# Kernel tuning notes

Measured on AMD Instinct MI355X. Metric: run time of the kernel, lower is better.

The kernel has to match this reference:

```python
import jax, jax.numpy as jnp
import numpy as np

PATCH = 11
STRIDE = 2
WIN_SIGMA = 1.5
C1 = 0.01 ** 2
C2 = 0.03 ** 2


def gauss_win():
    # 1D gaussian (matches _fspecial_gauss_1d) outer-producted to a 2D window
    # over the p*p patch pixels (separable SSIM window), flattened to (p*p,).
    coords = jnp.arange(PATCH, dtype=jnp.float32) - PATCH // 2
    g = jnp.exp(-(coords ** 2) / (2.0 * WIN_SIGMA ** 2))
    g = g / g.sum()
    return jnp.outer(g, g).reshape(-1)


def extract_patches(im):
    # im: (B,3,H,W) -> (B, n_patches, 3, p*p); feature dim of
    # conv_general_dilated_patches is channel-major (C, p, p).
    pat = jax.lax.conv_general_dilated_patches(
        im, (PATCH, PATCH), (STRIDE, STRIDE), 'VALID')  # (B, 3*p*p, H', W')
    B = im.shape[0]
    pat = pat.reshape(B, 3, PATCH * PATCH, -1)
    return jnp.transpose(pat, (0, 3, 1, 2))


def mmd_ssim(xp, yp, win):
    # xp: (M,3,pp), yp: (N,3,pp). Returns scalar MMD = s^T K s, where
    # K is the pairwise SSIM kernel matrix and s the scale vector.
    M, N = xp.shape[0], yp.shape[0]
    s = jnp.concatenate([jnp.full((N,), 1.0 / N, jnp.float32),
                         jnp.full((M,), -1.0 / M, jnp.float32)])
    X = jnp.concatenate([xp, yp], axis=0)
    X = (X + 1.0) / 2.0
    Xw = X * win                                   # (P,3,pp)
    mus = Xw.sum(-1)                               # (P,3)
    mus_sq = mus ** 2
    sigmas = (Xw * X).sum(-1) - mus_sq             # (P,3)
    sig_sum = sigmas[:, None] + sigmas[None, :]    # (P,P,3)
    mus_sum = mus_sq[:, None] + mus_sq[None, :]
    mus_mult = mus_sq[:, None] * mus_sq[None, :]
    sigmas_xy = jnp.einsum('icp,jcp->ijc', Xw, X) - mus_mult
    cs_map = (2.0 * sigmas_xy + C2) / (sig_sum + C2)
    ssim_map = (2.0 * mus_mult + C1) / (mus_sum + C1) * cs_map
    K = ssim_map.mean(-1)                          # (P,P)
    return s @ (K @ s)


def setup_inputs() -> dict:
    key = jax.random.key(0)
    kx, ky = jax.random.split(key)
    x = jax.random.normal(kx, (2, 3, 80, 80), dtype=jnp.float32)
    y = jax.random.normal(ky, (2, 3, 80, 80), dtype=jnp.float32)
    return {"x": x, "y": y}


def reference(x, y):
    win = gauss_win()
    xp = extract_patches(x)  # (B, P, 3, pp)
    yp = extract_patches(y)
    losses = jax.vmap(lambda a, b: mmd_ssim(a, b, win))(xp, yp)  # (B,)
    return losses.mean()  # batch_reduction='mean'
```

## Files before the change

kernel.cpp:

```cpp
#include <hip/hip_runtime.h>
#include <math.h>

#define PATCH   11
#define PP      121
#define NPX     35
#define NPATCH  1225
#define P2      2450
#define NC      3
#define NB      2
#define TILE    64
#define NT      39
#define NTP     ((NT*(NT+1))/2)
#define NROW    (NT*TILE)
#define KP      128
#define C1f     1.0e-4f
#define C2f     9.0e-4f

typedef _Float16 f16;
typedef __attribute__((ext_vector_type(8)))  _Float16 f16x8;
typedef __attribute__((ext_vector_type(16))) float    f32x16;

__device__ __forceinline__ void gload16(const void* g, void* l) {
    __builtin_amdgcn_global_load_lds((const __attribute__((address_space(1))) void*)(g),
                                     (__attribute__((address_space(3))) void*)(l),
                                     16, 0, 0);
}

__global__ __launch_bounds__(256) void extract_kernel(
        const float* __restrict__ x, const float* __restrict__ y,
        f16* __restrict__ Zh, f16* __restrict__ Zl,
        float* __restrict__ musq, float* __restrict__ sig,
        double* __restrict__ acc) {
    int w = threadIdx.x >> 6, lane = threadIdx.x & 63;
    int i = blockIdx.x * 4 + w;
    int c = blockIdx.y, b = blockIdx.z;
    if (threadIdx.x == 0 && blockIdx.x == 0 && c == 0 && b == 0) acc[0] = 0.0;
    if (i >= NROW) return;

    size_t rowbase = ((size_t)(b * NC + c) * NROW + i) * (size_t)KP;
    f16* zh = Zh + rowbase;
    f16* zl = Zl + rowbase;
    size_t sidx = (size_t)(b * NC + c) * NROW + i;

    if (i >= P2) {
        ((unsigned int*)zh)[lane] = 0u;
        ((unsigned int*)zl)[lane] = 0u;
        if (lane == 0) { musq[sidx] = 0.f; sig[sidx] = 0.f; }
        return;
    }

    float g1[PATCH]; float gs = 0.f;
#pragma unroll
    for (int k = 0; k < PATCH; k++) {
        float d = (float)(k - PATCH / 2);
        g1[k] = expf(-(d * d) / (2.0f * 1.5f * 1.5f));
        gs += g1[k];
    }
    float inv = 1.0f / gs;
    float inv2 = inv * inv;

    const float* img = (i < NPATCH) ? x : y;
    int ip = (i < NPATCH) ? i : i - NPATCH;
    int py = ip / NPX, px = ip - py * NPX;
    const float* base = img + ((size_t)(b * NC + c) * 80 + py * 2) * 80 + px * 2;

    float mu = 0.f, e2 = 0.f;
    f16 hv[2], lv[2];
#pragma unroll
    for (int q = 0; q < 2; q++) {
        int p = lane + q * 64;
        float z = 0.f;
        if (p < PP) {
            int r = p / PATCH, s = p - (p / PATCH) * PATCH;
            float wgt = g1[r] * g1[s] * inv2;
            float X = (base[r * 80 + s] + 1.0f) * 0.5f;
            mu = fmaf(wgt, X, mu);
            e2 = fmaf(wgt * X, X, e2);
            z = sqrtf(wgt) * X;
        }
        hv[q] = (f16)z;
        lv[q] = (f16)(z - (float)hv[q]);
    }
    zh[lane]      = hv[0];
    zh[lane + 64] = hv[1];
    zl[lane]      = lv[0];
    zl[lane + 64] = lv[1];

#pragma unroll
    for (int off = 32; off > 0; off >>= 1) {
        mu += __shfl_down(mu, off);
        e2 += __shfl_down(e2, off);
    }
    if (lane == 0) {
        float m2 = mu * mu;
        musq[sidx] = m2;
        sig [sidx] = e2 - m2;
    }
}

__device__ __forceinline__ f16x8 frag(const f16* arr, int r, int kb) {
    int off = r * 256 + (kb ^ ((r & 15) << 4));
    return *(const f16x8*)((const char*)arr + off);
}

__global__ __launch_bounds__(256) void pair_kernel(
        const f16* __restrict__ Zh, const f16* __restrict__ Zl,
        const float* __restrict__ musq, const float* __restrict__ sig,
        double* __restrict__ acc) {
    __shared__ __align__(16) f16 lds[4 * TILE * KP];

    int t = threadIdx.x;
    int lane = t & 63, w = t >> 6;
    int b = blockIdx.y;

    int l = blockIdx.x, ti = 0;
    while (l >= NT - ti) { l -= NT - ti; ti++; }
    int tj = ti + l;

    f16* A_h = lds;
    f16* A_l = lds + 8192;
    f16* B_h = lds + 16384;
    f16* B_l = lds + 24576;

    int wr = w >> 1, wc = w & 1;
    int rA = wr * 32 + (lane & 31);
    int rB = wc * 32 + (lane & 31);
    int kb0 = (lane >> 5) * 16;

    int soff[4];
#pragma unroll
    for (int q = 0; q < 4; q++) {
        int U = (w * 4 + q) * 64 + lane;
        int r = U >> 4, u = U & 15;
        soff[q] = r * 256 + (u ^ (r & 15)) * 16;
    }

    double local = 0.0;

    for (int c = 0; c < NC; c++) {
        __syncthreads();
        const char* gAh = (const char*)(Zh + ((size_t)(b * NC + c) * NROW + ti * TILE) * KP);
        const char* gAl = (const char*)(Zl + ((size_t)(b * NC + c) * NROW + ti * TILE) * KP);
        const char* gBh = (const char*)(Zh + ((size_t)(b * NC + c) * NROW + tj * TILE) * KP);
        const char* gBl = (const char*)(Zl + ((size_t)(b * NC + c) * NROW + tj * TILE) * KP);
#pragma unroll
        for (int q = 0; q < 4; q++) {
            int ldo = (w * 4 + q) * 512;
            gload16(gAh + soff[q], A_h + ldo);
            gload16(gAl + soff[q], A_l + ldo);
            gload16(gBh + soff[q], B_h + ldo);
            gload16(gBl + soff[q], B_l + ldo);
        }
        __syncthreads();

        f32x16 acc2 = {};
#pragma unroll
        for (int ks = 0; ks < 8; ks++) {
            int kb = ks * 32 + kb0;
            f16x8 ah = frag(A_h, rA, kb);
            f16x8 bh = frag(B_h, rB, kb);
            f16x8 al = frag(A_l, rA, kb);
            f16x8 bl = frag(B_l, rB, kb);
            acc2 = __builtin_amdgcn_mfma_f32_32x32x16_f16(ah, bh, acc2, 0, 0, 0);
            acc2 = __builtin_amdgcn_mfma_f32_32x32x16_f16(ah, bl, acc2, 0, 0, 0);
            acc2 = __builtin_amdgcn_mfma_f32_32x32x16_f16(al, bh, acc2, 0, 0, 0);
        }

        const float* msq = musq + (size_t)(b * NC + c) * NROW;
        const float* sg  = sig  + (size_t)(b * NC + c) * NROW;
        int row0 = ti * TILE + wr * 32;
        int col0 = tj * TILE + wc * 32;
        int gj = col0 + (lane & 31);
        float mj = msq[gj], sj = sg[gj];
        bool yj = gj < NPATCH;
#pragma unroll
        for (int reg = 0; reg < 16; reg++) {
            int gi = row0 + (reg & 3) + 8 * (reg >> 2) + 4 * (lane >> 5);
            float mi = msq[gi], si = sg[gi];
            float G   = acc2[reg];
            float mm  = mi * mj;
            float sxy = G - mm;
            float num = (2.f * mm + C1f) * (2.f * sxy + C2f);
            float den = (mi + mj + C1f) * (si + sj + C2f);
            float kv  = num * __builtin_amdgcn_rcpf(den);
            float wgt;
            if (ti == tj) wgt = (gj > gi) ? 2.f : ((gj == gi) ? 1.f : 0.f);
            else          wgt = 2.f;
            if (gi >= P2 || gj >= P2) wgt = 0.f;
            float sgn = ((gi < NPATCH) == yj) ? 1.f : -1.f;
            local += (double)(wgt * sgn * kv);
        }
    }

    __syncthreads();
#pragma unroll
    for (int off = 32; off > 0; off >>= 1)
        local += __shfl_down(local, off);
    double* red = (double*)lds;
    if (lane == 0) red[w] = local;
    __syncthreads();
    if (t == 0)
        atomicAdd(acc, red[0] + red[1] + red[2] + red[3]);
}

__global__ void finalize_kernel(const double* __restrict__ acc,
                                float* __restrict__ out) {
    if (threadIdx.x == 0 && blockIdx.x == 0)
        out[0] = (float)(acc[0] * (1.0 / (2.0 * 3.0 * (double)NPATCH * (double)NPATCH)));
}

extern "C" void kernel_launch(void* const* d_in, const int* in_sizes, int n_in,
                              void* d_out, int out_size, void* d_ws, size_t ws_size,
                              hipStream_t stream) {
    const float* x = (const float*)d_in[0];
    const float* y = (const float*)d_in[1];
    float* out = (float*)d_out;

    double* acc = (double*)d_ws;
    f16* Zh = (f16*)((char*)d_ws + 16);
    size_t zcnt = (size_t)NB * NC * NROW * KP;
    f16* Zl = Zh + zcnt;
    float* musq = (float*)(Zl + zcnt);
    float* sig  = musq + (size_t)NB * NC * NROW;

    dim3 g1((NROW + 3) / 4, NC, NB);
    extract_kernel<<<g1, 256, 0, stream>>>(x, y, Zh, Zl, musq, sig, acc);

    dim3 g2(NTP, NB);
    pair_kernel<<<g2, 256, 0, stream>>>(Zh, Zl, musq, sig, acc);

    finalize_kernel<<<1, 64, 0, stream>>>(acc, out);
}
```

Measured before the change: 103.5 us.

## Drop LDS staging; use k-chunk-major layout with direct global fragment loads

```diff
diff --git a/kernel.cpp b/kernel.cpp
--- a/kernel.cpp
+++ b/kernel.cpp
@@ -8,11 +8,12 @@
 #define P2      2450
 #define NC      3
 #define NB      2
-#define TILE    64
-#define NT      39
-#define NTP     ((NT*(NT+1))/2)
-#define NROW    (NT*TILE)
-#define KP      128
+#define NROW    2560
+#define NKC     16
+#define RT      128
+#define CT      64
+#define NSTRIP  (NROW/RT)
+#define NCT     (NROW/CT)
 #define C1f     1.0e-4f
 #define C2f     9.0e-4f
 
@@ -20,183 +21,131 @@
 typedef __attribute__((ext_vector_type(8)))  _Float16 f16x8;
 typedef __attribute__((ext_vector_type(16))) float    f32x16;
 
-__device__ __forceinline__ void gload16(const void* g, void* l) {
-    __builtin_amdgcn_global_load_lds((const __attribute__((address_space(1))) void*)(g),
-                                     (__attribute__((address_space(3))) void*)(l),
-                                     16, 0, 0);
-}
-
 __global__ __launch_bounds__(256) void extract_kernel(
         const float* __restrict__ x, const float* __restrict__ y,
         f16* __restrict__ Zh, f16* __restrict__ Zl,
-        float* __restrict__ musq, float* __restrict__ sig,
-        double* __restrict__ acc) {
-    int w = threadIdx.x >> 6, lane = threadIdx.x & 63;
-    int i = blockIdx.x * 4 + w;
+        float2* __restrict__ msig, double* __restrict__ acc) {
+    int t = threadIdx.x, lane = t & 63, w = t >> 6;
+    int i  = blockIdx.x * 16 + w * 4 + (lane >> 4);
+    int kc = lane & 15;
     int c = blockIdx.y, b = blockIdx.z;
-    if (threadIdx.x == 0 && blockIdx.x == 0 && c == 0 && b == 0) acc[0] = 0.0;
-    if (i >= NROW) return;
+    if (t == 0 && blockIdx.x == 0 && c == 0 && b == 0) acc[0] = 0.0;
 
-    size_t rowbase = ((size_t)(b * NC + c) * NROW + i) * (size_t)KP;
-    f16* zh = Zh + rowbase;
-    f16* zl = Zl + rowbase;
-    size_t sidx = (size_t)(b * NC + c) * NROW + i;
-
-    if (i >= P2) {
-        ((unsigned int*)zh)[lane] = 0u;
-        ((unsigned int*)zl)[lane] = 0u;
-        if (lane == 0) { musq[sidx] = 0.f; sig[sidx] = 0.f; }
-        return;
-    }
+    int bc = b * NC + c;
+    bool valid = (i < P2);
 
     float g1[PATCH]; float gs = 0.f;
 #pragma unroll
     for (int k = 0; k < PATCH; k++) {
         float d = (float)(k - PATCH / 2);
-        g1[k] = expf(-(d * d) / (2.0f * 1.5f * 1.5f));
+        g1[k] = expf(-(d * d) / 4.5f);
         gs += g1[k];
     }
-    float inv = 1.0f / gs;
-    float inv2 = inv * inv;
+    float inv2 = 1.0f / (gs * gs);
 
-    const float* img = (i < NPATCH) ? x : y;
-    int ip = (i < NPATCH) ? i : i - NPATCH;
-    int py = ip / NPX, px = ip - py * NPX;
-    const float* base = img + ((size_t)(b * NC + c) * 80 + py * 2) * 80 + px * 2;
+    const float* base = x;
+    if (valid) {
+        const float* img = (i < NPATCH) ? x : y;
+        int ip = (i < NPATCH) ? i : i - NPATCH;
+        int py = ip / NPX, px = ip - py * NPX;
+        base = img + ((size_t)bc * 80 + py * 2) * 80 + px * 2;
+    }
 
     float mu = 0.f, e2 = 0.f;
-    f16 hv[2], lv[2];
+    f16x8 hv = {}, lv = {};
 #pragma unroll
-    for (int q = 0; q < 2; q++) {
-        int p = lane + q * 64;
+    for (int q = 0; q < 8; q++) {
+        int p = kc * 8 + q;
         float z = 0.f;
-        if (p < PP) {
+        if (valid && p < PP) {
             int r = p / PATCH, s = p - (p / PATCH) * PATCH;
-            float wgt = g1[r] * g1[s] * inv2;
+            float wg = g1[r] * g1[s] * inv2;
             float X = (base[r * 80 + s] + 1.0f) * 0.5f;
-            mu = fmaf(wgt, X, mu);
-            e2 = fmaf(wgt * X, X, e2);
-            z = sqrtf(wgt) * X;
+            mu = fmaf(wg, X, mu);
+            e2 = fmaf(wg * X, X, e2);
+            z = sqrtf(wg) * X;
         }
-        hv[q] = (f16)z;
-        lv[q] = (f16)(z - (float)hv[q]);
+        f16 h = (f16)z;
+        hv[q] = h;
+        lv[q] = (f16)(z - (float)h);
     }
-    zh[lane]      = hv[0];
-    zh[lane + 64] = hv[1];
-    zl[lane]      = lv[0];
-    zl[lane + 64] = lv[1];
+    size_t off = (((size_t)bc * NKC + kc) * NROW + i) * 8;
+    *(f16x8*)(Zh + off) = hv;
+    *(f16x8*)(Zl + off) = lv;
 
 #pragma unroll
-    for (int off = 32; off > 0; off >>= 1) {
-        mu += __shfl_down(mu, off);
-        e2 += __shfl_down(e2, off);
+    for (int m = 1; m < 16; m <<= 1) {
+        mu += __shfl_xor(mu, m);
+        e2 += __shfl_xor(e2, m);
     }
-    if (lane == 0) {
+    if (kc == 0) {
         float m2 = mu * mu;
-        musq[sidx] = m2;
-        sig [sidx] = e2 - m2;
+        msig[(size_t)bc * NROW + i] = make_float2(m2, e2 - m2);
     }
-}
-
-__device__ __forceinline__ f16x8 frag(const f16* arr, int r, int kb) {
-    int off = r * 256 + (kb ^ ((r & 15) << 4));
-    return *(const f16x8*)((const char*)arr + off);
 }
 
 __global__ __launch_bounds__(256) void pair_kernel(
         const f16* __restrict__ Zh, const f16* __restrict__ Zl,
-        const float* __restrict__ musq, const float* __restrict__ sig,
-        double* __restrict__ acc) {
-    __shared__ __align__(16) f16 lds[4 * TILE * KP];
+        const float2* __restrict__ msig, double* __restrict__ acc) {
+    int tj = blockIdx.x, si = blockIdx.y, b = blockIdx.z;
+    if (tj < 2 * si) return;
 
-    int t = threadIdx.x;
-    int lane = t & 63, w = t >> 6;
-    int b = blockIdx.y;
-
-    int l = blockIdx.x, ti = 0;
-    while (l >= NT - ti) { l -= NT - ti; ti++; }
-    int tj = ti + l;
-
-    f16* A_h = lds;
-    f16* A_l = lds + 8192;
-    f16* B_h = lds + 16384;
-    f16* B_l = lds + 24576;
-
-    int wr = w >> 1, wc = w & 1;
-    int rA = wr * 32 + (lane & 31);
-    int rB = wc * 32 + (lane & 31);
-    int kb0 = (lane >> 5) * 16;
-
-    int soff[4];
-#pragma unroll
-    for (int q = 0; q < 4; q++) {
-        int U = (w * 4 + q) * 64 + lane;
-        int r = U >> 4, u = U & 15;
-        soff[q] = r * 256 + (u ^ (r & 15)) * 16;
-    }
+    int t = threadIdx.x, lane = t & 63, w = t >> 6;
+    int lr = lane & 31, hi = lane >> 5;
+    int R0 = si * RT + w * 32;
 
     double local = 0.0;
 
     for (int c = 0; c < NC; c++) {
-        __syncthreads();
-        const char* gAh = (const char*)(Zh + ((size_t)(b * NC + c) * NROW + ti * TILE) * KP);
-        const char* gAl = (const char*)(Zl + ((size_t)(b * NC + c) * NROW + ti * TILE) * KP);
-        const char* gBh = (const char*)(Zh + ((size_t)(b * NC + c) * NROW + tj * TILE) * KP);
-        const char* gBl = (const char*)(Zl + ((size_t)(b * NC + c) * NROW + tj * TILE) * KP);
+        int bc = b * NC + c;
+        const f16* zh = Zh + (size_t)bc * NKC * NROW * 8;
+        const f16* zl = Zl + (size_t)bc * NKC * NROW * 8;
+        const float2* ms = msig + (size_t)bc * NROW;
+
+        f16x8 Ah[8];
 #pragma unroll
-        for (int q = 0; q < 4; q++) {
-            int ldo = (w * 4 + q) * 512;
-            gload16(gAh + soff[q], A_h + ldo);
-            gload16(gAl + soff[q], A_l + ldo);
-            gload16(gBh + soff[q], B_h + ldo);
-            gload16(gBl + soff[q], B_l + ldo);
-        }
-        __syncthreads();
+        for (int ks = 0; ks < 8; ks++)
+            Ah[ks] = *(const f16x8*)(zh + ((size_t)(ks * 2 + hi) * NROW + R0 + lr) * 8);
 
-        f32x16 acc2 = {};
 #pragma unroll
-        for (int ks = 0; ks < 8; ks++) {
-            int kb = ks * 32 + kb0;
-            f16x8 ah = frag(A_h, rA, kb);
-            f16x8 bh = frag(B_h, rB, kb);
-            f16x8 al = frag(A_l, rA, kb);
-            f16x8 bl = frag(B_l, rB, kb);
-            acc2 = __builtin_amdgcn_mfma_f32_32x32x16_f16(ah, bh, acc2, 0, 0, 0);
-            acc2 = __builtin_amdgcn_mfma_f32_32x32x16_f16(ah, bl, acc2, 0, 0, 0);
-            acc2 = __builtin_amdgcn_mfma_f32_32x32x16_f16(al, bh, acc2, 0, 0, 0);
-        }
+        for (int cb = 0; cb < 2; cb++) {
+            int C0 = tj * CT + cb * 32;
+            f32x16 a = {};
+#pragma unroll
+            for (int ks = 0; ks < 8; ks++) {
+                size_t ko = (size_t)(ks * 2 + hi) * NROW;
+                f16x8 bh = *(const f16x8*)(zh + (ko + C0 + lr) * 8);
+                f16x8 bl = *(const f16x8*)(zl + (ko + C0 + lr) * 8);
+                f16x8 al = *(const f16x8*)(zl + (ko + R0 + lr) * 8);
+                a = __builtin_amdgcn_mfma_f32_32x32x16_f16(Ah[ks], bh, a, 0, 0, 0);
+                a = __builtin_amdgcn_mfma_f32_32x32x16_f16(Ah[ks], bl, a, 0, 0, 0);
+                a = __builtin_amdgcn_mfma_f32_32x32x16_f16(al,     bh, a, 0, 0, 0);
+            }
 
-        const float* msq = musq + (size_t)(b * NC + c) * NROW;
-        const float* sg  = sig  + (size_t)(b * NC + c) * NROW;
-        int row0 = ti * TILE + wr * 32;
-        int col0 = tj * TILE + wc * 32;
-        int gj = col0 + (lane & 31);
-        float mj = msq[gj], sj = sg[gj];
-        bool yj = gj < NPATCH;
+            int gj = C0 + lr;
+            float2 mj = ms[gj];
+            bool yj = gj < NPATCH;
 #pragma unroll
-        for (int reg = 0; reg < 16; reg++) {
-            int gi = row0 + (reg & 3) + 8 * (reg >> 2) + 4 * (lane >> 5);
-            float mi = msq[gi], si = sg[gi];
-            float G   = acc2[reg];
-            float mm  = mi * mj;
-            float sxy = G - mm;
-            float num = (2.f * mm + C1f) * (2.f * sxy + C2f);
-            float den = (mi + mj + C1f) * (si + sj + C2f);
-            float kv  = num * __builtin_amdgcn_rcpf(den);
-            float wgt;
-            if (ti == tj) wgt = (gj > gi) ? 2.f : ((gj == gi) ? 1.f : 0.f);
-            else          wgt = 2.f;
-            if (gi >= P2 || gj >= P2) wgt = 0.f;
-            float sgn = ((gi < NPATCH) == yj) ? 1.f : -1.f;
-            local += (double)(wgt * sgn * kv);
+            for (int reg = 0; reg < 16; reg++) {
+                int gi = R0 + (reg & 3) + 8 * (reg >> 2) + 4 * hi;
+                float2 mi = ms[gi];
+                float mm  = mi.x * mj.x;
+                float sxy = a[reg] - mm;
+                float num = (2.f * mm + C1f) * (2.f * sxy + C2f);
+                float den = (mi.x + mj.x + C1f) * (mi.y + mj.y + C2f);
+                float kv  = num * __builtin_amdgcn_rcpf(den);
+                float wgt = (gj > gi) ? 2.f : ((gj == gi) ? 1.f : 0.f);
+                if (gi >= P2 || gj >= P2) wgt = 0.f;
+                float sgn = ((gi < NPATCH) == yj) ? 1.f : -1.f;
+                local += (double)(wgt * sgn * kv);
+            }
         }
     }
 
-    __syncthreads();
 #pragma unroll
     for (int off = 32; off > 0; off >>= 1)
         local += __shfl_down(local, off);
-    double* red = (double*)lds;
+    __shared__ double red[4];
     if (lane == 0) red[w] = local;
     __syncthreads();
     if (t == 0)
@@ -218,16 +167,15 @@
 
     double* acc = (double*)d_ws;
     f16* Zh = (f16*)((char*)d_ws + 16);
-    size_t zcnt = (size_t)NB * NC * NROW * KP;
+    size_t zcnt = (size_t)NB * NC * NKC * NROW * 8;
     f16* Zl = Zh + zcnt;
-    float* musq = (float*)(Zl + zcnt);
-    float* sig  = musq + (size_t)NB * NC * NROW;
+    float2* msig = (float2*)(Zl + zcnt);
 
-    dim3 g1((NROW + 3) / 4, NC, NB);
-    extract_kernel<<<g1, 256, 0, stream>>>(x, y, Zh, Zl, musq, sig, acc);
+    dim3 g1(NROW / 16, NC, NB);
+    extract_kernel<<<g1, 256, 0, stream>>>(x, y, Zh, Zl, msig, acc);
 
-    dim3 g2(NTP, NB);
-    pair_kernel<<<g2, 256, 0, stream>>>(Zh, Zl, musq, sig, acc);
+    dim3 g2(NCT, NSTRIP, NB);
+    pair_kernel<<<g2, 256, 0, stream>>>(Zh, Zl, msig, acc);
 
     finalize_kernel<<<1, 64, 0, stream>>>(acc, out);
 }
```

After: 115.8 us. 1.12x slower.
